# Kernel tuning notes

Measured on AMD Instinct MI355X. Metric: run time of the kernel, lower is better.

## Reference

```python
import jax, jax.numpy as jnp
import numpy as np

IN_F = 1024
OUT_F = 4096
SEARCH_SPACE = [1, 2, 4, 8, 16]  # block sizes; powers of 2 dividing both dims, capped at 16


def circ_avg(W, bs):
    """Project W [out,in] onto block-circulant structure with block size bs.

    Equivalent to trans_to_cir_meng: within each (bs x bs) block, average each
    wrap-around diagonal and rebuild a circulant block C[k, j] = c[(k - j) % bs].
    """
    q, p = W.shape[0] // bs, W.shape[1] // bs
    t = W.reshape(q, bs, p, bs).transpose(0, 2, 1, 3)  # [q, p, bs, bs]
    i = jnp.arange(bs)
    # rot[..., i, j] = t[..., i, (i + j) % bs]  (rotate rows so diagonals align in columns)
    rot = t[:, :, i[:, None], (i[:, None] + i[None, :]) % bs]  # [q, p, bs, bs]
    c = rot.mean(axis=2)  # [q, p, bs]  mean over each diagonal
    # circulant block: w[..., k, j] = c[..., (k - j) % bs]
    w = c[:, :, (i[:, None] - i[None, :]) % bs]  # [q, p, bs, bs]
    return w.transpose(0, 2, 1, 3).reshape(W.shape)


def setup_inputs() -> dict:
    key = jax.random.key(0)
    k1, k2, k3, k4 = jax.random.split(key, 4)
    x = jax.random.normal(k1, (16, 512, IN_F), dtype=jnp.float32)
    weight = jax.random.normal(k2, (OUT_F, IN_F), dtype=jnp.float32) * 0.02
    alphas = jax.random.normal(k3, (len(SEARCH_SPACE),), dtype=jnp.float32)
    bias = jax.random.normal(k4, (OUT_F,), dtype=jnp.float32) * 0.02
    return {"x": x, "weight": weight, "alphas": alphas, "bias": bias}


def reference(x, weight, alphas, bias):
    # soft NAS mixture over block sizes (tau=1, soft mode)
    a = jax.nn.softmax(alphas)
    W = a[0] * weight  # block_size 1 == original weight
    for idx, bs in enumerate(SEARCH_SPACE[1:], start=1):
        W = W + a[idx] * circ_avg(weight, bs)
    # F.linear: y = x @ W^T + b
    return jnp.einsum("bsi,oi->bso", x, W) + bias
```

## Files before the change

kernel.cpp:

```cpp
#include <hip/hip_runtime.h>

typedef __bf16 bf16;
typedef __bf16 bf16x8 __attribute__((ext_vector_type(8)));
typedef float floatx4 __attribute__((ext_vector_type(4)));

#define IN_F  1024
#define OUT_F 4096
#define M_DIM 8192
#define K_DIM 1024
#define N_DIM 4096

__device__ __forceinline__ unsigned short f2bf(float f) {
    unsigned int u = __float_as_uint(f);
    u += 0x7FFFu + ((u >> 16) & 1u);
    return (unsigned short)(u >> 16);
}

__global__ __launch_bounds__(256) void build_w_kernel(
    const float* __restrict__ W, const float* __restrict__ alphas,
    unsigned short* __restrict__ Wb)
{
    __shared__ float Wl[16 * 256];

    const int t = threadIdx.x;
    const int rb = blockIdx.x >> 2;
    const int cb = blockIdx.x & 3;
    const int row0 = rb * 16, col0 = cb * 256;

    const float4* src = (const float4*)(W + (size_t)row0 * IN_F + col0);
    #pragma unroll
    for (int j = 0; j < 4; ++j) {
        const int idx = j * 256 + t;
        const int r = idx >> 6, c4 = idx & 63;
        ((float4*)Wl)[r * 64 + c4] = src[(size_t)r * 256 + c4];
    }

    float av[5];
    float mx = -1e30f;
    #pragma unroll
    for (int j = 0; j < 5; ++j) { av[j] = alphas[j]; mx = fmaxf(mx, av[j]); }
    float s = 0.f;
    #pragma unroll
    for (int j = 0; j < 5; ++j) { av[j] = __expf(av[j] - mx); s += av[j]; }
    const float inv = 1.f / s;
    #pragma unroll
    for (int j = 0; j < 5; ++j) av[j] *= inv;

    __syncthreads();

    const int k  = t >> 4;
    const int jj = t & 15;
    unsigned short ov[16];

    #pragma unroll
    for (int jb = 0; jb < 16; ++jb) {
        const int jr = (jb + k) & 15;
        const int j  = jr * 16 + jj;
        float acc = av[0] * Wl[k * 256 + j];
        #pragma unroll
        for (int e = 1; e <= 4; ++e) {
            const int bs   = 1 << e;
            const int mask = bs - 1;
            const int ol = k & ~mask;
            const int il = j & ~mask;
            const int d  = (k - j) & mask;
            float ssum = 0.f;
            #pragma unroll
            for (int r = 0; r < bs; ++r)
                ssum += Wl[(ol + r) * 256 + il + ((r + d) & mask)];
            acc += av[e] * (1.0f / (float)bs) * ssum;
        }
        ov[jb] = f2bf(acc);
    }

    __syncthreads();
    unsigned short* Wls = (unsigned short*)Wl;
    #pragma unroll
    for (int jb = 0; jb < 16; ++jb) {
        const int jr = (jb + k) & 15;
        Wls[k * 256 + jr * 16 + jj] = ov[jb];
    }
    __syncthreads();

    const int kr = t >> 4, cg = t & 15;
    const uint4* p = (const uint4*)(Wls + kr * 256 + cg * 16);
    uint4* dst = (uint4*)(Wb + (size_t)(row0 + kr) * IN_F + col0 + cg * 16);
    dst[0] = p[0];
    dst[1] = p[1];
}

__global__ __launch_bounds__(256) void cvt_x_kernel(
    const float* __restrict__ x, uint4* __restrict__ xb)
{
    const int t = blockIdx.x * 256 + threadIdx.x;
    const float4* xv = (const float4*)x;
    const float4 v0 = xv[2 * t];
    const float4 v1 = xv[2 * t + 1];
    uint4 o;
    o.x = (unsigned)f2bf(v0.x) | ((unsigned)f2bf(v0.y) << 16);
    o.y = (unsigned)f2bf(v0.z) | ((unsigned)f2bf(v0.w) << 16);
    o.z = (unsigned)f2bf(v1.x) | ((unsigned)f2bf(v1.y) << 16);
    o.w = (unsigned)f2bf(v1.z) | ((unsigned)f2bf(v1.w) << 16);
    xb[t] = o;
}

__global__ __launch_bounds__(256, 2) void gemm_bt_kernel(
    const bf16* __restrict__ A, const bf16* __restrict__ B,
    const float* __restrict__ bias, float* __restrict__ C)
{
    constexpr int N = N_DIM, K = K_DIM;
    constexpr int TM = 256, TN = 128, TK = 64;

    __shared__ __align__(16) bf16 Bs[TN * TK];

    const int t    = threadIdx.x;
    const int w    = t >> 6;
    const int l    = t & 63;
    const int quad = l >> 4;
    const int l16  = l & 15;
    const int x7   = l16 & 7;

    const int nb = N / TN;
    const int bm = blockIdx.x / nb;
    const int bn = blockIdx.x % nb;
    const int wm = w * 64;

    floatx4 acc[4][8] = {};

    int crow[4], ccol[4], loff[4];
    #pragma unroll
    for (int q = 0; q < 4; ++q) {
        const int chunk = q * 256 + t;
        crow[q] = chunk >> 3;
        ccol[q] = (((chunk & 7) ^ ((chunk >> 3) & 7)) * 8);
        loff[q] = (q * 256 + (t & ~63)) * 8;
    }

    const bf16* Abase = A + (size_t)(bm * TM + wm) * K;
    const bf16* Bbase = B + (size_t)bn * TN * K;

    #pragma unroll 1
    for (int kt = 0; kt < K; kt += TK) {
        #pragma unroll
        for (int q = 0; q < 4; ++q) {
            __builtin_amdgcn_global_load_lds(
                (const __attribute__((address_space(1))) void*)(Bbase + (size_t)crow[q] * K + kt + ccol[q]),
                (__attribute__((address_space(3))) void*)(Bs + loff[q]), 16, 0, 0);
        }
        bf16x8 af[2][4];
        #pragma unroll
        for (int ks = 0; ks < 2; ++ks)
            #pragma unroll
            for (int mt = 0; mt < 4; ++mt)
                af[ks][mt] = *(const bf16x8*)(Abase + (size_t)(mt * 16 + l16) * K
                                              + kt + ks * 32 + quad * 8);
        __syncthreads();

        #pragma unroll
        for (int ks = 0; ks < 2; ++ks) {
            bf16x8 bfr[8];
            const int kx = ((ks * 4 + quad) ^ x7) * 8;
            #pragma unroll
            for (int nt = 0; nt < 8; ++nt)
                bfr[nt] = *(const bf16x8*)(Bs + (nt * 16 + l16) * TK + kx);
            #pragma unroll
            for (int mt = 0; mt < 4; ++mt)
                #pragma unroll
                for (int nt = 0; nt < 8; ++nt)
                    acc[mt][nt] = __builtin_amdgcn_mfma_f32_16x16x32_bf16(
                        af[ks][mt], bfr[nt], acc[mt][nt], 0, 0, 0);
        }
        __syncthreads();
    }

    float bv[8];
    #pragma unroll
    for (int nt = 0; nt < 8; ++nt)
        bv[nt] = bias[bn * TN + nt * 16 + l16];

    float* Cbase = C + (size_t)(bm * TM + wm) * N + bn * TN;
    #pragma unroll
    for (int mt = 0; mt < 4; ++mt) {
        #pragma unroll
        for (int r = 0; r < 4; ++r) {
            float* crowp = Cbase + (size_t)(mt * 16 + quad * 4 + r) * N;
            #pragma unroll
            for (int nt = 0; nt < 8; ++nt)
                crowp[nt * 16 + l16] = acc[mt][nt][r] + bv[nt];
        }
    }
}

extern "C" void kernel_launch(void* const* d_in, const int* in_sizes, int n_in,
                              void* d_out, int out_size, void* d_ws, size_t ws_size,
                              hipStream_t stream) {
    const float* x      = (const float*)d_in[0];
    const float* weight = (const float*)d_in[1];
    const float* alphas = (const float*)d_in[2];
    const float* bias   = (const float*)d_in[3];
    float* out = (float*)d_out;

    unsigned short* Wb = (unsigned short*)d_ws;
    unsigned short* Xb = (unsigned short*)((char*)d_ws + (size_t)OUT_F * IN_F * 2);

    build_w_kernel<<<(OUT_F / 16) * (IN_F / 256), 256, 0, stream>>>(weight, alphas, Wb);
    cvt_x_kernel<<<(M_DIM * K_DIM / 8) / 256, 256, 0, stream>>>(x, (uint4*)Xb);

    const int grid = (M_DIM / 256) * (N_DIM / 128);
    gemm_bt_kernel<<<grid, 256, 0, stream>>>((const bf16*)Xb, (const bf16*)Wb, bias, out);
}
```

Before: 251.3 us.

## Double-buffer B tile in LDS and prefetch next A/B tiles into registers

Replaces the single-buffered direct global-to-LDS loads of the B tile with register-staged loads into a double-buffered LDS tile. The next K-step's A fragments and B chunks are prefetched while MFMAs on the current step run, and each iteration now needs one barrier instead of two. The aim is to hide global memory latency behind compute. In exchange it uses more LDS and more registers, which could lower occupancy under launch bounds of 2 blocks per CU.

```diff
diff --git a/kernel.cpp b/kernel.cpp
--- a/kernel.cpp
+++ b/kernel.cpp
@@ -111,7 +111,7 @@
     constexpr int N = N_DIM, K = K_DIM;
     constexpr int TM = 256, TN = 128, TK = 64;
 
-    __shared__ __align__(16) bf16 Bs[TN * TK];
+    __shared__ __align__(16) bf16 Bs[2 * TN * TK];
 
     const int t    = threadIdx.x;
     const int w    = t >> 6;
@@ -127,50 +127,89 @@
 
     floatx4 acc[4][8] = {};
 
-    int crow[4], ccol[4], loff[4];
+    const bf16* Bp[4];
+    int wdst[4];
     #pragma unroll
     for (int q = 0; q < 4; ++q) {
         const int chunk = q * 256 + t;
-        crow[q] = chunk >> 3;
-        ccol[q] = (((chunk & 7) ^ ((chunk >> 3) & 7)) * 8);
-        loff[q] = (q * 256 + (t & ~63)) * 8;
-    }
-
-    const bf16* Abase = A + (size_t)(bm * TM + wm) * K;
-    const bf16* Bbase = B + (size_t)bn * TN * K;
+        const int row = chunk >> 3, kc = chunk & 7;
+        Bp[q]   = B + (size_t)(bn * TN + row) * K + kc * 8;
+        wdst[q] = row * TK + (kc ^ (row & 7)) * 8;
+    }
+
+    const bf16* Ap = A + (size_t)(bm * TM + wm + l16) * K + quad * 8;
+
+    bf16x8 af0[4], af1[4];
+    uint4 breg[4];
+
+    #pragma unroll
+    for (int q = 0; q < 4; ++q) breg[q] = *(const uint4*)(Bp[q]);
+    #pragma unroll
+    for (int mt = 0; mt < 4; ++mt)
+        af0[mt] = *(const bf16x8*)(Ap + (size_t)mt * 16 * K);
+    #pragma unroll
+    for (int mt = 0; mt < 4; ++mt)
+        af1[mt] = *(const bf16x8*)(Ap + (size_t)mt * 16 * K + 32);
+    #pragma unroll
+    for (int q = 0; q < 4; ++q) *(uint4*)(Bs + wdst[q]) = breg[q];
+    asm volatile("s_waitcnt lgkmcnt(0)\ns_barrier" ::: "memory");
+
+    const bf16* bs_r = Bs;
+    bf16* bs_w = Bs + TN * TK;
 
     #pragma unroll 1
     for (int kt = 0; kt < K; kt += TK) {
-        #pragma unroll
-        for (int q = 0; q < 4; ++q) {
-            __builtin_amdgcn_global_load_lds(
-                (const __attribute__((address_space(1))) void*)(Bbase + (size_t)crow[q] * K + kt + ccol[q]),
-                (__attribute__((address_space(3))) void*)(Bs + loff[q]), 16, 0, 0);
-        }
-        bf16x8 af[2][4];
-        #pragma unroll
-        for (int ks = 0; ks < 2; ++ks)
-            #pragma unroll
-            for (int mt = 0; mt < 4; ++mt)
-                af[ks][mt] = *(const bf16x8*)(Abase + (size_t)(mt * 16 + l16) * K
-                                              + kt + ks * 32 + quad * 8);
-        __syncthreads();
-
-        #pragma unroll
-        for (int ks = 0; ks < 2; ++ks) {
+        const bool nl = (kt + TK) < K;
+
+        if (nl) {
+            #pragma unroll
+            for (int q = 0; q < 4; ++q)
+                breg[q] = *(const uint4*)(Bp[q] + kt + TK);
+        }
+
+        {
             bf16x8 bfr[8];
-            const int kx = ((ks * 4 + quad) ^ x7) * 8;
+            const int kx = (quad ^ x7) * 8;
             #pragma unroll
             for (int nt = 0; nt < 8; ++nt)
-                bfr[nt] = *(const bf16x8*)(Bs + (nt * 16 + l16) * TK + kx);
+                bfr[nt] = *(const bf16x8*)(bs_r + (nt * 16 + l16) * TK + kx);
             #pragma unroll
             for (int mt = 0; mt < 4; ++mt)
                 #pragma unroll
                 for (int nt = 0; nt < 8; ++nt)
                     acc[mt][nt] = __builtin_amdgcn_mfma_f32_16x16x32_bf16(
-                        af[ks][mt], bfr[nt], acc[mt][nt], 0, 0, 0);
-        }
-        __syncthreads();
+                        af0[mt], bfr[nt], acc[mt][nt], 0, 0, 0);
+        }
+        if (nl) {
+            #pragma unroll
+            for (int mt = 0; mt < 4; ++mt)
+                af0[mt] = *(const bf16x8*)(Ap + (size_t)mt * 16 * K + kt + TK);
+        }
+
+        {
+            bf16x8 bfr[8];
+            const int kx = ((4 + quad) ^ x7) * 8;
+            #pragma unroll
+            for (int nt = 0; nt < 8; ++nt)
+                bfr[nt] = *(const bf16x8*)(bs_r + (nt * 16 + l16) * TK + kx);
+            #pragma unroll
+            for (int mt = 0; mt < 4; ++mt)
+                #pragma unroll
+                for (int nt = 0; nt < 8; ++nt)
+                    acc[mt][nt] = __builtin_amdgcn_mfma_f32_16x16x32_bf16(
+                        af1[mt], bfr[nt], acc[mt][nt], 0, 0, 0);
+        }
+        if (nl) {
+            #pragma unroll
+            for (int mt = 0; mt < 4; ++mt)
+                af1[mt] = *(const bf16x8*)(Ap + (size_t)mt * 16 * K + kt + TK + 32);
+            #pragma unroll
+            for (int q = 0; q < 4; ++q)
+                *(uint4*)(bs_w + wdst[q]) = breg[q];
+        }
+
+        asm volatile("s_waitcnt lgkmcnt(0)\ns_barrier" ::: "memory");
+        const bf16* tmp = bs_r; bs_r = bs_w; bs_w = (bf16*)tmp;
     }
 
     float bv[8];
```

After: 295.1 us. 1.17x slower.

## Double-buffer B tile in LDS and prefetch A fragments in GEMM loop

Applied to the files above, without the earlier changes.

The GEMM main loop now uses two LDS buffers for the B tile and two register sets for the A fragments. The loop is unrolled by two K-steps, so the next tile's global-to-LDS copy and A loads are issued before the current tile's MFMAs run. This is meant to hide global memory latency behind compute and cut the barriers per K-step from two to one. In exchange it doubles LDS use for B and adds roughly 32 more VGPRs for the A fragments, which may put pressure on the two-blocks-per-CU occupancy target.

```diff
diff --git a/kernel.cpp b/kernel.cpp
--- a/kernel.cpp
+++ b/kernel.cpp
@@ -111,7 +111,8 @@
     constexpr int N = N_DIM, K = K_DIM;
     constexpr int TM = 256, TN = 128, TK = 64;
 
-    __shared__ __align__(16) bf16 Bs[TN * TK];
+    __shared__ __align__(16) bf16 Bs0[TN * TK];
+    __shared__ __align__(16) bf16 Bs1[TN * TK];
 
     const int t    = threadIdx.x;
     const int w    = t >> 6;
@@ -136,47 +137,92 @@
         loff[q] = (q * 256 + (t & ~63)) * 8;
     }
 
-    const bf16* Abase = A + (size_t)(bm * TM + wm) * K;
     const bf16* Bbase = B + (size_t)bn * TN * K;
-
-    #pragma unroll 1
-    for (int kt = 0; kt < K; kt += TK) {
-        #pragma unroll
-        for (int q = 0; q < 4; ++q) {
-            __builtin_amdgcn_global_load_lds(
-                (const __attribute__((address_space(1))) void*)(Bbase + (size_t)crow[q] * K + kt + ccol[q]),
-                (__attribute__((address_space(3))) void*)(Bs + loff[q]), 16, 0, 0);
-        }
-        bf16x8 af[2][4];
-        #pragma unroll
-        for (int ks = 0; ks < 2; ++ks)
-            #pragma unroll
-            for (int mt = 0; mt < 4; ++mt)
-                af[ks][mt] = *(const bf16x8*)(Abase + (size_t)(mt * 16 + l16) * K
-                                              + kt + ks * 32 + quad * 8);
-        __syncthreads();
-
-        #pragma unroll
-        for (int ks = 0; ks < 2; ++ks) {
-            bf16x8 bfr[8];
-            const int kx = ((ks * 4 + quad) ^ x7) * 8;
-            #pragma unroll
-            for (int nt = 0; nt < 8; ++nt)
-                bfr[nt] = *(const bf16x8*)(Bs + (nt * 16 + l16) * TK + kx);
-            #pragma unroll
-            for (int mt = 0; mt < 4; ++mt)
-                #pragma unroll
-                for (int nt = 0; nt < 8; ++nt)
-                    acc[mt][nt] = __builtin_amdgcn_mfma_f32_16x16x32_bf16(
-                        af[ks][mt], bfr[nt], acc[mt][nt], 0, 0, 0);
-        }
-        __syncthreads();
-    }
+    const bf16* Ap    = A + (size_t)(bm * TM + wm + l16) * K + quad * 8;
+
+    bf16x8 afA[2][4], afB[2][4];
 
     float bv[8];
     #pragma unroll
     for (int nt = 0; nt < 8; ++nt)
         bv[nt] = bias[bn * TN + nt * 16 + l16];
+
+    #pragma unroll
+    for (int q = 0; q < 4; ++q)
+        __builtin_amdgcn_global_load_lds(
+            (const __attribute__((address_space(1))) void*)(Bbase + (size_t)crow[q] * K + ccol[q]),
+            (__attribute__((address_space(3))) void*)(Bs0 + loff[q]), 16, 0, 0);
+    #pragma unroll
+    for (int ks = 0; ks < 2; ++ks)
+        #pragma unroll
+        for (int mt = 0; mt < 4; ++mt)
+            afA[ks][mt] = *(const bf16x8*)(Ap + (size_t)mt * 16 * K + ks * 32);
+    __syncthreads();
+
+    #pragma unroll 1
+    for (int kt = 0; kt < K; kt += 2 * TK) {
+        {
+            const int kn = kt + TK;
+            #pragma unroll
+            for (int q = 0; q < 4; ++q)
+                __builtin_amdgcn_global_load_lds(
+                    (const __attribute__((address_space(1))) void*)(Bbase + (size_t)crow[q] * K + kn + ccol[q]),
+                    (__attribute__((address_space(3))) void*)(Bs1 + loff[q]), 16, 0, 0);
+            #pragma unroll
+            for (int ks = 0; ks < 2; ++ks)
+                #pragma unroll
+                for (int mt = 0; mt < 4; ++mt)
+                    afB[ks][mt] = *(const bf16x8*)(Ap + (size_t)mt * 16 * K + kn + ks * 32);
+
+            #pragma unroll
+            for (int ks = 0; ks < 2; ++ks) {
+                bf16x8 bfr[8];
+                const int kx = ((ks * 4 + quad) ^ x7) * 8;
+                #pragma unroll
+                for (int nt = 0; nt < 8; ++nt)
+                    bfr[nt] = *(const bf16x8*)(Bs0 + (nt * 16 + l16) * TK + kx);
+                #pragma unroll
+                for (int mt = 0; mt < 4; ++mt)
+                    #pragma unroll
+                    for (int nt = 0; nt < 8; ++nt)
+                        acc[mt][nt] = __builtin_amdgcn_mfma_f32_16x16x32_bf16(
+                            afA[ks][mt], bfr[nt], acc[mt][nt], 0, 0, 0);
+            }
+            __syncthreads();
+        }
+
+        {
+            const int kn = kt + 2 * TK;
+            if (kn < K) {
+                #pragma unroll
+                for (int q = 0; q < 4; ++q)
+                    __builtin_amdgcn_global_load_lds(
+                        (const __attribute__((address_space(1))) void*)(Bbase + (size_t)crow[q] * K + kn + ccol[q]),
+                        (__attribute__((address_space(3))) void*)(Bs0 + loff[q]), 16, 0, 0);
+                #pragma unroll
+                for (int ks = 0; ks < 2; ++ks)
+                    #pragma unroll
+                    for (int mt = 0; mt < 4; ++mt)
+                        afA[ks][mt] = *(const bf16x8*)(Ap + (size_t)mt * 16 * K + kn + ks * 32);
+            }
+
+            #pragma unroll
+            for (int ks = 0; ks < 2; ++ks) {
+                bf16x8 bfr[8];
+                const int kx = ((ks * 4 + quad) ^ x7) * 8;
+                #pragma unroll
+                for (int nt = 0; nt < 8; ++nt)
+                    bfr[nt] = *(const bf16x8*)(Bs1 + (nt * 16 + l16) * TK + kx);
+                #pragma unroll
+                for (int mt = 0; mt < 4; ++mt)
+                    #pragma unroll
+                    for (int nt = 0; nt < 8; ++nt)
+                        acc[mt][nt] = __builtin_amdgcn_mfma_f32_16x16x32_bf16(
+                            afB[ks][mt], bfr[nt], acc[mt][nt], 0, 0, 0);
+            }
+            __syncthreads();
+        }
+    }
 
     float* Cbase = C + (size_t)(bm * TM + wm) * N + bn * TN;
     #pragma unroll
```

Measured after the change: 327.8 us. +30.4%, slower.
